# Optimization experiments

Hardware: AMD Instinct MI355X
Metric: run time of the kernel (lower is better)

## Reference

```python
import jax, jax.numpy as jnp
import numpy as np

N = 50000        # n_nodes
E = 640000       # n_edges
D = 128          # d_model (in_dim == out_dim)
H = 8            # num_heads
DH = D // H      # head dim = 16
EPS = 1e-5


def _batchnorm(x, g, b):
    # BatchNorm1d, training-mode batch statistics (biased variance)
    mu = jnp.mean(x, axis=0)
    var = jnp.mean((x - mu) ** 2, axis=0)
    return (x - mu) * jax.lax.rsqrt(var + EPS) * g + b


def setup_inputs() -> dict:
    key = jax.random.key(0)
    ks = jax.random.split(key, 16)
    s = 0.05
    h = jax.random.normal(ks[0], (N, D), jnp.float32)
    src = jax.random.randint(ks[1], (E,), 0, N)
    # guarantee every node has >= 1 incoming edge (avoids z == 0)
    dst = jnp.concatenate([jnp.arange(N), jax.random.randint(ks[2], (E - N,), 0, N)])
    return {
        "h": h,
        "src": src,
        "dst": dst,
        "WQ": jax.random.normal(ks[3], (D, D), jnp.float32) * s,
        "WK": jax.random.normal(ks[4], (D, D), jnp.float32) * s,
        "WV": jax.random.normal(ks[5], (D, D), jnp.float32) * s,
        "WO": jax.random.normal(ks[6], (D, D), jnp.float32) * s,
        "bO": jnp.zeros((D,), jnp.float32),
        "W1": jax.random.normal(ks[7], (2 * D, D), jnp.float32) * s,
        "b1": jnp.zeros((2 * D,), jnp.float32),
        "W2": jax.random.normal(ks[8], (D, 2 * D), jnp.float32) * s,
        "b2": jnp.zeros((D,), jnp.float32),
        "bn1_g": jnp.ones((D,), jnp.float32),
        "bn1_b": jnp.zeros((D,), jnp.float32),
        "bn2_g": jnp.ones((D,), jnp.float32),
        "bn2_b": jnp.zeros((D,), jnp.float32),
    }


def reference(h, src, dst, WQ, WK, WV, WO, bO, W1, b1, W2, b2, bn1_g, bn1_b, bn2_g, bn2_b):
    n = h.shape[0]
    # projections -> [N, H, DH]
    Q = (h @ WQ.T).reshape(n, H, DH)
    K = (h @ WK.T).reshape(n, H, DH)
    V = (h @ WV.T).reshape(n, H, DH)
    # per-edge score: sum(K[src] * Q[dst]) -> [E, H]; clamp/exp (scaled_exp)
    score = jnp.sum(K[src] * Q[dst], axis=-1) / np.sqrt(DH)
    score = jnp.exp(jnp.clip(score, -5.0, 5.0))
    # scatter-sum weighted values and normalizers to destination nodes
    wV = jax.ops.segment_sum(V[src] * score[..., None], dst, num_segments=n)  # [N,H,DH]
    z = jax.ops.segment_sum(score, dst, num_segments=n)                       # [N,H]
    attn = (wV / z[..., None]).reshape(n, D)
    # O projection + residual + BN1
    h1 = _batchnorm(h + (attn @ WO.T + bO), bn1_g, bn1_b)
    # FFN + residual + BN2
    f = jax.nn.relu(h1 @ W1.T + b1) @ W2.T + b2
    return _batchnorm(h1 + f, bn2_g, bn2_b)
```

## Files before the change

### kernel.cpp

```cpp
#include <hip/hip_runtime.h>
#include <math.h>


#define ND128 16384
typedef _Float16 f16;
typedef __attribute__((ext_vector_type(8))) _Float16 h8;
typedef __attribute__((ext_vector_type(4))) _Float16 h4;
typedef __attribute__((ext_vector_type(2))) _Float16 h2;
typedef __attribute__((ext_vector_type(4))) float f4;

__global__ __launch_bounds__(256) void k_prep(
    const float* __restrict__ h, f16* __restrict__ hb,
    const float* __restrict__ WQ, const float* __restrict__ WK,
    const float* __restrict__ WV, const float* __restrict__ WO,
    const float* __restrict__ W2,
    f16* __restrict__ Wqb, f16* __restrict__ Wkb,
    f16* __restrict__ Wvb, f16* __restrict__ Wob, f16* __restrict__ W2b,
    float* __restrict__ bn, int* __restrict__ cursor, int N)
{
    const int slab = blockIdx.x;
    const int tid = threadIdx.x;
    if (tid < 128) {
        int ci = slab * 128 + tid;
        if (ci < N) cursor[ci] = 0;
    }
    if (slab == 6) { bn[tid] = 0.f; bn[tid + 256] = 0.f; }
#pragma unroll
    for (int it = 0; it < 8; ++it) {
        int cid = it * 256 + tid;
        int lane = cid & 63;
        int m = (cid >> 6) & 7;
        int kb = cid >> 9;
        int row = slab * 128 + m * 16 + (lane & 15);
        int col = kb * 32 + (lane >> 4) * 8;
        f16 o8[8];
        if (row < N) {
            const float* p = h + (size_t)row * 128 + col;
            float4 f0 = *(const float4*)p;
            float4 f1 = *(const float4*)(p + 4);
            o8[0] = (f16)f0.x; o8[1] = (f16)f0.y; o8[2] = (f16)f0.z; o8[3] = (f16)f0.w;
            o8[4] = (f16)f1.x; o8[5] = (f16)f1.y; o8[6] = (f16)f1.z; o8[7] = (f16)f1.w;
        } else {
#pragma unroll
            for (int j = 0; j < 8; ++j) o8[j] = (f16)0.f;
        }
        *(h8*)(hb + (size_t)slab * ND128 + (size_t)cid * 8) = *(const h8*)o8;
    }
    if (slab < 6) {
        const float* Wsrc; f16* dst; int K, base;
        if (slab < 4) {
            Wsrc = slab == 0 ? WQ : slab == 1 ? WK : slab == 2 ? WV : WO;
            dst  = slab == 0 ? Wqb : slab == 1 ? Wkb : slab == 2 ? Wvb : Wob;
            K = 128; base = 0;
        } else {
            Wsrc = W2; dst = W2b; K = 256; base = (slab - 4) * 2048;
        }
#pragma unroll
        for (int it = 0; it < 8; ++it) {
            int cid = base + it * 256 + tid;
            int lane = cid & 63;
            int kb, nt;
            if (K == 128) { kb = (cid >> 6) & 3; nt = cid >> 8; }
            else          { kb = (cid >> 6) & 7; nt = cid >> 9; }
            int row = nt * 16 + (lane & 15);
            int col = kb * 32 + (lane >> 4) * 8;
            const float* p = Wsrc + (size_t)row * K + col;
            f16 o8[8];
#pragma unroll
            for (int j = 0; j < 8; ++j) o8[j] = (f16)p[j];
            *(h8*)(dst + (size_t)cid * 8) = *(const h8*)o8;
        }
    }
}

__global__ __launch_bounds__(256) void k_qkv(
    const f16* __restrict__ hb, const f16* __restrict__ Wqb,
    const f16* __restrict__ Wkb, const f16* __restrict__ Wvb,
    f16* __restrict__ Qb, f16* __restrict__ Kb, f16* __restrict__ Vb, int N)
{
    const int slab = blockIdx.x;
    const int w = threadIdx.x >> 6, lane = threadIdx.x & 63;
    const f16* __restrict__ Wb = blockIdx.y == 0 ? Wqb : blockIdx.y == 1 ? Wkb : Wvb;
    f16* __restrict__ Ob = blockIdx.y == 0 ? Qb : blockIdx.y == 1 ? Kb : Vb;
    const f16* A = hb + (size_t)slab * ND128;

    h8 bfr[2][4];
#pragma unroll
    for (int nt = 0; nt < 2; ++nt)
#pragma unroll
        for (int kb = 0; kb < 4; ++kb)
            bfr[nt][kb] = *(const h8*)(Wb + (size_t)(((2 * w + nt) * 4 + kb) * 64 + lane) * 8);

    f4 acc[8][2];
    f4 zero = {0.f, 0.f, 0.f, 0.f};
#pragma unroll
    for (int m = 0; m < 8; ++m) { acc[m][0] = zero; acc[m][1] = zero; }

#pragma unroll
    for (int m = 0; m < 8; ++m) {
#pragma unroll
        for (int kb = 0; kb < 4; ++kb) {
            h8 a = *(const h8*)(A + (size_t)((kb * 8 + m) * 64 + lane) * 8);
            acc[m][0] = __builtin_amdgcn_mfma_f32_16x16x32_f16(bfr[0][kb], a, acc[m][0], 0, 0, 0);
            acc[m][1] = __builtin_amdgcn_mfma_f32_16x16x32_f16(bfr[1][kb], a, acc[m][1], 0, 0, 0);
        }
    }

    const int rl = lane & 15, quad = lane >> 4;
#pragma unroll
    for (int m = 0; m < 8; ++m) {
        int gr = slab * 128 + m * 16 + rl;
        if (gr < N) {
#pragma unroll
            for (int nt = 0; nt < 2; ++nt) {
                h4 o;
                o[0] = (f16)acc[m][nt][0]; o[1] = (f16)acc[m][nt][1];
                o[2] = (f16)acc[m][nt][2]; o[3] = (f16)acc[m][nt][3];
                *(h4*)(Ob + (size_t)gr * 128 + w * 32 + nt * 16 + quad * 4) = o;
            }
        }
    }
}

__global__ __launch_bounds__(256) void k_hist(
    const int* __restrict__ dst, int* __restrict__ cursor, int E)
{
    int e = blockIdx.x * 256 + threadIdx.x;
    if (e < E) atomicAdd(&cursor[dst[e]], 1);
}

__global__ __launch_bounds__(256) void k_scanA(
    const int* __restrict__ cnt, int* __restrict__ bsum, int N)
{
    const int t = threadIdx.x;
    int base = blockIdx.x * 2048 + t * 8;
    int s = 0;
#pragma unroll
    for (int j = 0; j < 8; ++j) {
        int idx = base + j;
        if (idx < N) s += cnt[idx];
    }
#pragma unroll
    for (int off = 32; off; off >>= 1) s += __shfl_down(s, off, 64);
    __shared__ int ws4[4];
    if ((t & 63) == 0) ws4[t >> 6] = s;
    __syncthreads();
    if (t == 0) bsum[blockIdx.x] = ws4[0] + ws4[1] + ws4[2] + ws4[3];
}

__global__ __launch_bounds__(256) void k_scanC(
    const int* __restrict__ cnt, const int* __restrict__ bsum,
    int* __restrict__ rowptr, int* __restrict__ cursor, int N, int nsb)
{
    const int t = threadIdx.x, b = blockIdx.x;
    __shared__ int sboff;
    if (t == 0) {
        int r = 0;
        for (int i2 = 0; i2 < b; ++i2) r += bsum[i2];
        sboff = r;
    }
    if (t == 64 && b == nsb - 1) {
        int r = 0;
        for (int i2 = 0; i2 < nsb; ++i2) r += bsum[i2];
        rowptr[N] = r;
    }
    int base = b * 2048 + t * 8;
    int loc[8];
    int s = 0;
#pragma unroll
    for (int j = 0; j < 8; ++j) {
        int idx = base + j;
        loc[j] = (idx < N) ? cnt[idx] : 0;
        s += loc[j];
    }
    __shared__ int part[256];
    part[t] = s;
    __syncthreads();
    for (int off = 1; off < 256; off <<= 1) {
        int v = (t >= off) ? part[t - off] : 0;
        __syncthreads();
        part[t] += v;
        __syncthreads();
    }
    int run = sboff + (t ? part[t - 1] : 0);
#pragma unroll
    for (int j = 0; j < 8; ++j) {
        int idx = base + j;
        if (idx < N) { rowptr[idx] = run; cursor[idx] = run; run += loc[j]; }
    }
}

__global__ __launch_bounds__(256) void k_scatter(
    const int* __restrict__ src, const int* __restrict__ dst,
    int* __restrict__ cursor, int* __restrict__ csr_src, int E)
{
    int e = blockIdx.x * 256 + threadIdx.x;
    if (e < E) {
        int pos = atomicAdd(&cursor[dst[e]], 1);
        csr_src[pos] = src[e];
    }
}

__global__ __launch_bounds__(256) void k_attn(
    const f16* __restrict__ Qb, const f16* __restrict__ Kb,
    const f16* __restrict__ Vb,
    const int* __restrict__ rowptr, const int* __restrict__ csr_src,
    f16* __restrict__ attnf, int N)
{
    const int node = blockIdx.x * 4 + (threadIdx.x >> 6);
    const int lane = threadIdx.x & 63;
    if (node >= N) return;
    const int beg = rowptr[node], end = rowptr[node + 1];
    const h2 q2 = ((const h2*)(Qb + (size_t)node * 128))[lane];
    h2 accA = {(f16)0.f, (f16)0.f};
    h2 accB = {(f16)0.f, (f16)0.f};
    float zA = 0.f, zB = 0.f;
    int i = beg;
    for (; i + 3 < end; i += 4) {
        int s0 = csr_src[i], s1 = csr_src[i + 1];
        int s2 = csr_src[i + 2], s3 = csr_src[i + 3];
        h2 k0 = ((const h2*)(Kb + (size_t)s0 * 128))[lane];
        h2 k1 = ((const h2*)(Kb + (size_t)s1 * 128))[lane];
        h2 k2 = ((const h2*)(Kb + (size_t)s2 * 128))[lane];
        h2 k3 = ((const h2*)(Kb + (size_t)s3 * 128))[lane];
        h2 v0 = ((const h2*)(Vb + (size_t)s0 * 128))[lane];
        h2 v1 = ((const h2*)(Vb + (size_t)s1 * 128))[lane];
        h2 v2 = ((const h2*)(Vb + (size_t)s2 * 128))[lane];
        h2 v3 = ((const h2*)(Vb + (size_t)s3 * 128))[lane];
        float p0 = __builtin_amdgcn_fdot2(q2, k0, 0.f, false);
        float p1 = __builtin_amdgcn_fdot2(q2, k1, 0.f, false);
        float p2 = __builtin_amdgcn_fdot2(q2, k2, 0.f, false);
        float p3 = __builtin_amdgcn_fdot2(q2, k3, 0.f, false);
        p0 += __shfl_xor(p0, 4, 8); p1 += __shfl_xor(p1, 4, 8);
        p2 += __shfl_xor(p2, 4, 8); p3 += __shfl_xor(p3, 4, 8);
        p0 += __shfl_xor(p0, 2, 8); p1 += __shfl_xor(p1, 2, 8);
        p2 += __shfl_xor(p2, 2, 8); p3 += __shfl_xor(p3, 2, 8);
        p0 += __shfl_xor(p0, 1, 8); p1 += __shfl_xor(p1, 1, 8);
        p2 += __shfl_xor(p2, 1, 8); p3 += __shfl_xor(p3, 1, 8);
        float sc0 = __expf(fminf(fmaxf(p0 * 0.25f, -5.f), 5.f));
        float sc1 = __expf(fminf(fmaxf(p1 * 0.25f, -5.f), 5.f));
        float sc2 = __expf(fminf(fmaxf(p2 * 0.25f, -5.f), 5.f));
        float sc3 = __expf(fminf(fmaxf(p3 * 0.25f, -5.f), 5.f));
        h2 h0 = {(f16)sc0, (f16)sc0}, h1v = {(f16)sc1, (f16)sc1};
        h2 h2v = {(f16)sc2, (f16)sc2}, h3 = {(f16)sc3, (f16)sc3};
        accA = v0 * h0 + accA;  accB = v1 * h1v + accB;
        accA = v2 * h2v + accA; accB = v3 * h3 + accB;
        zA += sc0 + sc2; zB += sc1 + sc3;
    }
    for (; i < end; ++i) {
        int s0 = csr_src[i];
        h2 k0 = ((const h2*)(Kb + (size_t)s0 * 128))[lane];
        h2 v0 = ((const h2*)(Vb + (size_t)s0 * 128))[lane];
        float p0 = __builtin_amdgcn_fdot2(q2, k0, 0.f, false);
        p0 += __shfl_xor(p0, 4, 8); p0 += __shfl_xor(p0, 2, 8); p0 += __shfl_xor(p0, 1, 8);
        float sc0 = __expf(fminf(fmaxf(p0 * 0.25f, -5.f), 5.f));
        h2 h0 = {(f16)sc0, (f16)sc0};
        accA = v0 * h0 + accA;
        zA += sc0;
    }
    h2 acc2 = accA + accB;
    float z = zA + zB;
    float inv = 1.f / z;
    h2 o2 = {(f16)((float)acc2.x * inv), (f16)((float)acc2.y * inv)};
    int slab = node >> 7, m = (node >> 4) & 7, lr = node & 15;
    int kb = lane >> 4, quad2 = (lane & 15) >> 2, j = (lane & 3) * 2;
    *(h2*)(attnf + (size_t)slab * ND128 +
           (size_t)(((kb * 8 + m) * 64 + lr + 16 * quad2) * 8 + j)) = o2;
}

__global__ __launch_bounds__(256) void k_oproj(
    const f16* __restrict__ attnf, const f16* __restrict__ Wob,
    const float* __restrict__ h, const float* __restrict__ bO,
    f16* __restrict__ t1b, float* __restrict__ bn, int N)
{
    __shared__ float csum[128], csq[128];
    const int tid = threadIdx.x, slab = blockIdx.x;
    const int w = tid >> 6, lane = tid & 63;
    if (tid < 128) { csum[tid] = 0.f; csq[tid] = 0.f; }
    __syncthreads();
    const f16* A = attnf + (size_t)slab * ND128;

    h8 bfr[2][4];
#pragma unroll
    for (int nt = 0; nt < 2; ++nt)
#pragma unroll
        for (int kb = 0; kb < 4; ++kb)
            bfr[nt][kb] = *(const h8*)(Wob + (size_t)(((2 * w + nt) * 4 + kb) * 64 + lane) * 8);

    f4 acc[8][2];
    f4 zero = {0.f, 0.f, 0.f, 0.f};
#pragma unroll
    for (int m = 0; m < 8; ++m) { acc[m][0] = zero; acc[m][1] = zero; }
#pragma unroll
    for (int m = 0; m < 8; ++m) {
#pragma unroll
        for (int kb = 0; kb < 4; ++kb) {
            h8 a = *(const h8*)(A + (size_t)((kb * 8 + m) * 64 + lane) * 8);
            acc[m][0] = __builtin_amdgcn_mfma_f32_16x16x32_f16(bfr[0][kb], a, acc[m][0], 0, 0, 0);
            acc[m][1] = __builtin_amdgcn_mfma_f32_16x16x32_f16(bfr[1][kb], a, acc[m][1], 0, 0, 0);
        }
    }

    const int rl = lane & 15, quad = lane >> 4;
    float4 bo[2];
#pragma unroll
    for (int nt = 0; nt < 2; ++nt)
        bo[nt] = *(const float4*)(bO + w * 32 + nt * 16 + quad * 4);
    float pcs[2][4], pcq[2][4];
#pragma unroll
    for (int nt = 0; nt < 2; ++nt)
#pragma unroll
        for (int r = 0; r < 4; ++r) { pcs[nt][r] = 0.f; pcq[nt][r] = 0.f; }

#pragma unroll
    for (int m = 0; m < 8; ++m) {
        int gr = slab * 128 + m * 16 + rl;
        if (gr < N) {
#pragma unroll
            for (int nt = 0; nt < 2; ++nt) {
                int col0 = w * 32 + nt * 16 + quad * 4;
                float4 hv = *(const float4*)(h + (size_t)gr * 128 + col0);
                float v0 = acc[m][nt][0] + hv.x + bo[nt].x;
                float v1 = acc[m][nt][1] + hv.y + bo[nt].y;
                float v2 = acc[m][nt][2] + hv.z + bo[nt].z;
                float v3 = acc[m][nt][3] + hv.w + bo[nt].w;
                h4 o; o[0] = (f16)v0; o[1] = (f16)v1; o[2] = (f16)v2; o[3] = (f16)v3;
                *(h4*)(t1b + (size_t)slab * ND128 +
                       (size_t)(((w * 8 + m) * 64 + (nt * 2 + (quad >> 1)) * 16 + rl) * 8 +
                                (quad & 1) * 4)) = o;
                pcs[nt][0] += v0; pcq[nt][0] += v0 * v0;
                pcs[nt][1] += v1; pcq[nt][1] += v1 * v1;
                pcs[nt][2] += v2; pcq[nt][2] += v2 * v2;
                pcs[nt][3] += v3; pcq[nt][3] += v3 * v3;
            }
        }
    }
#pragma unroll
    for (int nt = 0; nt < 2; ++nt)
#pragma unroll
        for (int r = 0; r < 4; ++r) {
            float s = pcs[nt][r], q = pcq[nt][r];
            s += __shfl_xor(s, 8, 16); q += __shfl_xor(q, 8, 16);
            s += __shfl_xor(s, 4, 16); q += __shfl_xor(q, 4, 16);
            s += __shfl_xor(s, 2, 16); q += __shfl_xor(q, 2, 16);
            s += __shfl_xor(s, 1, 16); q += __shfl_xor(q, 1, 16);
            if (rl == 0) {
                int cl = w * 32 + nt * 16 + quad * 4 + r;
                atomicAdd(&csum[cl], s);
                atomicAdd(&csq[cl], q);
            }
        }
    __syncthreads();
    if (tid < 128) {
        atomicAdd(bn + tid, csum[tid]);
        atomicAdd(bn + 128 + tid, csq[tid]);
    }
}

__global__ __launch_bounds__(128) void k_fold1(
    const float* __restrict__ bn, const float* __restrict__ g1,
    const float* __restrict__ bb1, const float* __restrict__ W1,
    const float* __restrict__ b1, f16* __restrict__ W1b,
    float* __restrict__ badj, float* __restrict__ sfold,
    float* __restrict__ bfold, int N)
{
    const int o = blockIdx.x, i = threadIdx.x;
    float invN = 1.f / (float)N;
    float mu = bn[i] * invN;
    float var = bn[128 + i] * invN - mu * mu;
    float s = g1[i] * rsqrtf(var + 1e-5f);
    float bb = bb1[i] - mu * s;
    if (o == 0) { sfold[i] = s; bfold[i] = bb; }
    float wv = W1[(size_t)o * 128 + i];
    __shared__ float red[128];
    red[i] = wv * bb;
    const int nt = o >> 4, lanelow = o & 15;
    const int kb = i >> 5, quad = (i >> 3) & 3, j = i & 7;
    W1b[(size_t)(((nt * 4 + kb) * 64 + lanelow + 16 * quad) * 8 + j)] = (f16)(wv * s);
    __syncthreads();
#pragma unroll
    for (int off = 64; off; off >>= 1) {
        if (i < off) red[i] += red[i + off];
        __syncthreads();
    }
    if (i == 0) badj[o] = b1[o] + red[0];
}

__global__ __launch_bounds__(256) void k_ffn1(
    const f16* __restrict__ t1b, const f16* __restrict__ W1b,
    const float* __restrict__ badj, f16* __restrict__ ub, int N)
{
    const int slab = blockIdx.x, ch = blockIdx.y;
    const int w = threadIdx.x >> 6, lane = threadIdx.x & 63;
    const f16* A = t1b + (size_t)slab * ND128;

    h8 bfr[2][4];
#pragma unroll
    for (int nt = 0; nt < 2; ++nt)
#pragma unroll
        for (int kb = 0; kb < 4; ++kb) {
            int ntg = ch * 8 + 2 * w + nt;
            bfr[nt][kb] = *(const h8*)(W1b + (size_t)((ntg * 4 + kb) * 64 + lane) * 8);
        }

    f4 acc[8][2];
    f4 zero = {0.f, 0.f, 0.f, 0.f};
#pragma unroll
    for (int m = 0; m < 8; ++m) { acc[m][0] = zero; acc[m][1] = zero; }
#pragma unroll
    for (int m = 0; m < 8; ++m) {
#pragma unroll
        for (int kb = 0; kb < 4; ++kb) {
            h8 a = *(const h8*)(A + (size_t)((kb * 8 + m) * 64 + lane) * 8);
            acc[m][0] = __builtin_amdgcn_mfma_f32_16x16x32_f16(bfr[0][kb], a, acc[m][0], 0, 0, 0);
            acc[m][1] = __builtin_amdgcn_mfma_f32_16x16x32_f16(bfr[1][kb], a, acc[m][1], 0, 0, 0);
        }
    }

    const int rl = lane & 15, quad = lane >> 4;
    const int kbu = ch * 4 + w;
    float4 ba[2];
#pragma unroll
    for (int nt = 0; nt < 2; ++nt)
        ba[nt] = *(const float4*)(badj + ch * 128 + w * 32 + nt * 16 + quad * 4);
#pragma unroll
    for (int m = 0; m < 8; ++m) {
        int gr = slab * 128 + m * 16 + rl;
        if (gr < N) {
#pragma unroll
            for (int nt = 0; nt < 2; ++nt) {
                h4 o;
                o[0] = (f16)fmaxf(acc[m][nt][0] + ba[nt].x, 0.f);
                o[1] = (f16)fmaxf(acc[m][nt][1] + ba[nt].y, 0.f);
                o[2] = (f16)fmaxf(acc[m][nt][2] + ba[nt].z, 0.f);
                o[3] = (f16)fmaxf(acc[m][nt][3] + ba[nt].w, 0.f);
                *(h4*)(ub + (size_t)slab * 32768 +
                       (size_t)(((kbu * 8 + m) * 64 + (nt * 2 + (quad >> 1)) * 16 + rl) * 8 +
                                (quad & 1) * 4)) = o;
            }
        }
    }
}

__global__ __launch_bounds__(256) void k_ffn2(
    const f16* __restrict__ ub, const f16* __restrict__ W2b,
    const f16* __restrict__ t1b,
    const float* __restrict__ sfold, const float* __restrict__ bfold,
    const float* __restrict__ b2, float* __restrict__ out,
    float* __restrict__ bn, int N)
{
    __shared__ float csum[128], csq[128], sS[128], sB[128];
    const int tid = threadIdx.x, slab = blockIdx.x;
    const int w = tid >> 6, lane = tid & 63;
    if (tid < 128) {
        csum[tid] = 0.f; csq[tid] = 0.f;
        sS[tid] = sfold[tid]; sB[tid] = bfold[tid] + b2[tid];
    }
    __syncthreads();
    const f16* A = ub + (size_t)slab * 32768;
    const f16* T1 = t1b + (size_t)slab * ND128;

    h8 bfr[2][8];
#pragma unroll
    for (int nt = 0; nt < 2; ++nt)
#pragma unroll
        for (int kb = 0; kb < 8; ++kb)
            bfr[nt][kb] = *(const h8*)(W2b + (size_t)(((2 * w + nt) * 8 + kb) * 64 + lane) * 8);

    f4 acc[8][2];
    f4 zero = {0.f, 0.f, 0.f, 0.f};
#pragma unroll
    for (int m = 0; m < 8; ++m) { acc[m][0] = zero; acc[m][1] = zero; }
#pragma unroll
    for (int m = 0; m < 8; ++m) {
#pragma unroll
        for (int kb = 0; kb < 8; ++kb) {
            h8 a = *(const h8*)(A + (size_t)((kb * 8 + m) * 64 + lane) * 8);
            acc[m][0] = __builtin_amdgcn_mfma_f32_16x16x32_f16(bfr[0][kb], a, acc[m][0], 0, 0, 0);
            acc[m][1] = __builtin_amdgcn_mfma_f32_16x16x32_f16(bfr[1][kb], a, acc[m][1], 0, 0, 0);
        }
    }

    const int rl = lane & 15, quad = lane >> 4;
    float pcs[2][4], pcq[2][4];
#pragma unroll
    for (int nt = 0; nt < 2; ++nt)
#pragma unroll
        for (int r = 0; r < 4; ++r) { pcs[nt][r] = 0.f; pcq[nt][r] = 0.f; }

#pragma unroll
    for (int m = 0; m < 8; ++m) {
        int gr = slab * 128 + m * 16 + rl;
        if (gr < N) {
#pragma unroll
            for (int nt = 0; nt < 2; ++nt) {
                int col0 = w * 32 + nt * 16 + quad * 4;
                h4 t1v = *(const h4*)(T1 +
                    (size_t)(((w * 8 + m) * 64 + (nt * 2 + (quad >> 1)) * 16 + rl) * 8 +
                             (quad & 1) * 4));
                float4 ss = *(const float4*)&sS[col0];
                float4 sb = *(const float4*)&sB[col0];
                float4 o;
                o.x = acc[m][nt][0] + fmaf(ss.x, (float)t1v[0], sb.x);
                o.y = acc[m][nt][1] + fmaf(ss.y, (float)t1v[1], sb.y);
                o.z = acc[m][nt][2] + fmaf(ss.z, (float)t1v[2], sb.z);
                o.w = acc[m][nt][3] + fmaf(ss.w, (float)t1v[3], sb.w);
                *(float4*)(out + (size_t)gr * 128 + col0) = o;
                pcs[nt][0] += o.x; pcq[nt][0] += o.x * o.x;
                pcs[nt][1] += o.y; pcq[nt][1] += o.y * o.y;
                pcs[nt][2] += o.z; pcq[nt][2] += o.z * o.z;
                pcs[nt][3] += o.w; pcq[nt][3] += o.w * o.w;
            }
        }
    }
#pragma unroll
    for (int nt = 0; nt < 2; ++nt)
#pragma unroll
        for (int r = 0; r < 4; ++r) {
            float s = pcs[nt][r], q = pcq[nt][r];
            s += __shfl_xor(s, 8, 16); q += __shfl_xor(q, 8, 16);
            s += __shfl_xor(s, 4, 16); q += __shfl_xor(q, 4, 16);
            s += __shfl_xor(s, 2, 16); q += __shfl_xor(q, 2, 16);
            s += __shfl_xor(s, 1, 16); q += __shfl_xor(q, 1, 16);
            if (rl == 0) {
                int cl = w * 32 + nt * 16 + quad * 4 + r;
                atomicAdd(&csum[cl], s);
                atomicAdd(&csq[cl], q);
            }
        }
    __syncthreads();
    if (tid < 128) {
        atomicAdd(bn + 256 + tid, csum[tid]);
        atomicAdd(bn + 384 + tid, csq[tid]);
    }
}

__global__ __launch_bounds__(256) void k_bn2(
    float* __restrict__ out, const float* __restrict__ bn,
    const float* __restrict__ g2, const float* __restrict__ bb2, int N)
{
    __shared__ float sS[128], sB[128];
    const int tid = threadIdx.x;
    if (tid < 128) {
        float invN = 1.f / (float)N;
        float mu = bn[256 + tid] * invN;
        float var = bn[384 + tid] * invN - mu * mu;
        float scl = g2[tid] * rsqrtf(var + 1e-5f);
        sS[tid] = scl;
        sB[tid] = bb2[tid] - mu * scl;
    }
    __syncthreads();
    size_t idx = (size_t)blockIdx.x * 256 + tid;
    size_t total = (size_t)N * 32;
    if (idx < total) {
        int c0 = (int)((idx * 4) & 127);
        float4 v = *(const float4*)(out + idx * 4);
        v.x = fmaf(v.x, sS[c0 + 0], sB[c0 + 0]);
        v.y = fmaf(v.y, sS[c0 + 1], sB[c0 + 1]);
        v.z = fmaf(v.z, sS[c0 + 2], sB[c0 + 2]);
        v.w = fmaf(v.w, sS[c0 + 3], sB[c0 + 3]);
        *(float4*)(out + idx * 4) = v;
    }
}

extern "C" void kernel_launch(void* const* d_in, const int* in_sizes, int n_in,
                              void* d_out, int out_size, void* d_ws, size_t ws_size,
                              hipStream_t stream)
{
    const float* h   = (const float*)d_in[0];
    const int*   src = (const int*)d_in[1];
    const int*   dst = (const int*)d_in[2];
    const float* WQ  = (const float*)d_in[3];
    const float* WK  = (const float*)d_in[4];
    const float* WV  = (const float*)d_in[5];
    const float* WO  = (const float*)d_in[6];
    const float* bO  = (const float*)d_in[7];
    const float* W1  = (const float*)d_in[8];
    const float* b1  = (const float*)d_in[9];
    const float* W2  = (const float*)d_in[10];
    const float* b2  = (const float*)d_in[11];
    const float* g1  = (const float*)d_in[12];
    const float* bb1 = (const float*)d_in[13];
    const float* g2  = (const float*)d_in[14];
    const float* bb2 = (const float*)d_in[15];
    float* out = (float*)d_out;

    int N = in_sizes[0] / 128;
    int E = in_sizes[1];
    const int slabs = (N + 127) / 128;
    const int nsb = (N + 2047) / 2048;
    const size_t B1 = (size_t)slabs * 32768;

    char* Wp = (char*)d_ws;
    f16* hb  = (f16*)Wp;
    f16* Qb  = (f16*)(Wp + B1);
    f16* Kb  = (f16*)(Wp + 2 * B1);
    f16* Vb  = (f16*)(Wp + 3 * B1);
    f16* t1b = (f16*)(Wp + 3 * B1);
    f16* ub  = (f16*)(Wp + B1);
    const size_t base = 4 * B1;
    f16* Wqb = (f16*)(Wp + base);
    f16* Wkb = (f16*)(Wp + base + 32768);
    f16* Wvb = (f16*)(Wp + base + 65536);
    f16* Wob = (f16*)(Wp + base + 98304);
    f16* W1b = (f16*)(Wp + base + 131072);
    f16* W2b = (f16*)(Wp + base + 196608);
    float* badj  = (float*)(Wp + base + 262144);
    float* sfold = (float*)(Wp + base + 263168);
    float* bfold = (float*)(Wp + base + 263680);
    float* bn    = (float*)(Wp + base + 264192);
    int* cursor  = (int*)(Wp + base + 266240);
    int* rowptr  = (int*)(Wp + base + 266240 + (size_t)N * 4);
    int* csr     = (int*)(Wp + base + 266240 + (size_t)N * 8 + 8);
    int* bsum    = (int*)((char*)csr + (size_t)E * 4);

    k_prep<<<slabs, 256, 0, stream>>>(h, hb, WQ, WK, WV, WO, W2,
                                      Wqb, Wkb, Wvb, Wob, W2b, bn, cursor, N);
    k_qkv<<<dim3(slabs, 3), 256, 0, stream>>>(hb, Wqb, Wkb, Wvb, Qb, Kb, Vb, N);
    k_hist<<<(E + 255) / 256, 256, 0, stream>>>(dst, cursor, E);
    k_scanA<<<nsb, 256, 0, stream>>>(cursor, bsum, N);
    k_scanC<<<nsb, 256, 0, stream>>>(cursor, bsum, rowptr, cursor, N, nsb);
    k_scatter<<<(E + 255) / 256, 256, 0, stream>>>(src, dst, cursor, csr, E);
    k_attn<<<(N + 3) / 4, 256, 0, stream>>>(Qb, Kb, Vb, rowptr, csr, hb, N);
    k_oproj<<<slabs, 256, 0, stream>>>(hb, Wob, h, bO, t1b, bn, N);
    k_fold1<<<256, 128, 0, stream>>>(bn, g1, bb1, W1, b1, W1b, badj, sfold, bfold, N);
    k_ffn1<<<dim3(slabs, 2), 256, 0, stream>>>(t1b, W1b, badj, ub, N);
    k_ffn2<<<slabs, 256, 0, stream>>>(ub, W2b, t1b, sfold, bfold, b2, out, bn, N);
    k_bn2<<<(int)(((size_t)N * 32 + 255) / 256), 256, 0, stream>>>(out, bn, g2, bb2, N);
}
```

Before: 331.9 us.

## Store K and V in fp8 and fuse h conversion into QKV projection

K and V are now written as fp8 (e4m3) and decoded to fp32 inside the edge-gather attention kernel. This halves the bytes fetched per gathered edge, which is where the random-access memory traffic is concentrated. The h-to-fp16 conversion moves into a single fused QKV kernel that loads each slab of h once and computes all three projections, removing the separate hb buffer and the three-way grid. The cost is reduced precision on K and V, which may push error past tolerance, plus extra decode arithmetic in the attention loop.

```diff
diff --git a/kernel.cpp b/kernel.cpp
--- a/kernel.cpp
+++ b/kernel.cpp
@@ -8,115 +8,177 @@
 typedef __attribute__((ext_vector_type(4))) _Float16 h4;
 typedef __attribute__((ext_vector_type(2))) _Float16 h2;
 typedef __attribute__((ext_vector_type(4))) float f4;
+typedef __attribute__((ext_vector_type(2))) float ff2;
+
+__device__ __forceinline__ ff2 fp8x2_dec(unsigned v) {
+#if __has_builtin(__builtin_amdgcn_cvt_pk_f32_fp8)
+    return __builtin_amdgcn_cvt_pk_f32_fp8((int)v, false);
+#else
+    ff2 r;
+    unsigned b0 = v & 0xffu, b1 = (v >> 8) & 0xffu;
+    {
+        unsigned e = (b0 >> 3) & 15u, m = b0 & 7u;
+        float x = e ? __uint_as_float(((e + 120u) << 23) | (m << 20)) : (float)m * 0.001953125f;
+        r.x = (b0 & 0x80u) ? -x : x;
+    }
+    {
+        unsigned e = (b1 >> 3) & 15u, m = b1 & 7u;
+        float x = e ? __uint_as_float(((e + 120u) << 23) | (m << 20)) : (float)m * 0.001953125f;
+        r.y = (b1 & 0x80u) ? -x : x;
+    }
+    return r;
+#endif
+}
+
+#if !__has_builtin(__builtin_amdgcn_cvt_pk_fp8_f32)
+__device__ __forceinline__ unsigned char fp8_1(float f) {
+    float a = fabsf(f);
+    unsigned sg = (__float_as_uint(f) >> 31) << 7;
+    if (a >= 448.f) return (unsigned char)(sg | 0x7E);
+    if (a < 0.0009765625f) return (unsigned char)sg;
+    int E; float m = frexpf(a, &E);
+    if (E - 1 < -6) {
+        int q = (int)rintf(a * 512.f);
+        if (q > 7) return (unsigned char)(sg | 0x08);
+        return (unsigned char)(sg | q);
+    }
+    int q = (int)rintf(m * 16.f);
+    if (q == 16) { q = 8; E += 1; }
+    int Ef = E - 1 + 7;
+    if (Ef > 15) return (unsigned char)(sg | 0x7E);
+    return (unsigned char)(sg | (Ef << 3) | (q - 8));
+}
+#endif
+
+__device__ __forceinline__ unsigned fp8_pack4(float a0, float a1, float a2, float a3) {
+#if __has_builtin(__builtin_amdgcn_cvt_pk_fp8_f32)
+    int pk = __builtin_amdgcn_cvt_pk_fp8_f32(a0, a1, 0, false);
+    pk = __builtin_amdgcn_cvt_pk_fp8_f32(a2, a3, pk, true);
+    return (unsigned)pk;
+#else
+    return (unsigned)fp8_1(a0) | ((unsigned)fp8_1(a1) << 8) |
+           ((unsigned)fp8_1(a2) << 16) | ((unsigned)fp8_1(a3) << 24);
+#endif
+}
 
 __global__ __launch_bounds__(256) void k_prep(
-    const float* __restrict__ h, f16* __restrict__ hb,
     const float* __restrict__ WQ, const float* __restrict__ WK,
     const float* __restrict__ WV, const float* __restrict__ WO,
     const float* __restrict__ W2,
     f16* __restrict__ Wqb, f16* __restrict__ Wkb,
     f16* __restrict__ Wvb, f16* __restrict__ Wob, f16* __restrict__ W2b,
-    float* __restrict__ bn, int* __restrict__ cursor, int N)
-{
-    const int slab = blockIdx.x;
-    const int tid = threadIdx.x;
+    float* __restrict__ bn)
+{
+    const int b = blockIdx.x, tid = threadIdx.x;
+    if (b == 0) { bn[tid] = 0.f; bn[tid + 256] = 0.f; }
+    const float* Wsrc; f16* dst; int K, base;
+    if (b < 4) {
+        Wsrc = b == 0 ? WQ : b == 1 ? WK : b == 2 ? WV : WO;
+        dst  = b == 0 ? Wqb : b == 1 ? Wkb : b == 2 ? Wvb : Wob;
+        K = 128; base = 0;
+    } else {
+        Wsrc = W2; dst = W2b; K = 256; base = (b - 4) * 2048;
+    }
+#pragma unroll
+    for (int it = 0; it < 8; ++it) {
+        int cid = base + it * 256 + tid;
+        int lane = cid & 63;
+        int kb, nt;
+        if (K == 128) { kb = (cid >> 6) & 3; nt = cid >> 8; }
+        else          { kb = (cid >> 6) & 7; nt = cid >> 9; }
+        int row = nt * 16 + (lane & 15);
+        int col = kb * 32 + (lane >> 4) * 8;
+        const float* p = Wsrc + (size_t)row * K + col;
+        f16 o8[8];
+#pragma unroll
+        for (int j = 0; j < 8; ++j) o8[j] = (f16)p[j];
+        *(h8*)(dst + (size_t)cid * 8) = *(const h8*)o8;
+    }
+}
+
+__global__ __launch_bounds__(256) void k_qkvF(
+    const float* __restrict__ h,
+    const f16* __restrict__ Wqb, const f16* __restrict__ Wkb, const f16* __restrict__ Wvb,
+    f16* __restrict__ Qb, unsigned char* __restrict__ Kb8, unsigned char* __restrict__ Vb8,
+    int* __restrict__ cursor, int N)
+{
+    const int slab = blockIdx.x, tid = threadIdx.x;
+    const int w = tid >> 6, lane = tid & 63;
+    const int rl = lane & 15, quad = lane >> 4;
     if (tid < 128) {
         int ci = slab * 128 + tid;
         if (ci < N) cursor[ci] = 0;
     }
-    if (slab == 6) { bn[tid] = 0.f; bn[tid + 256] = 0.f; }
-#pragma unroll
-    for (int it = 0; it < 8; ++it) {
-        int cid = it * 256 + tid;
-        int lane = cid & 63;
-        int m = (cid >> 6) & 7;
-        int kb = cid >> 9;
-        int row = slab * 128 + m * 16 + (lane & 15);
-        int col = kb * 32 + (lane >> 4) * 8;
-        f16 o8[8];
-        if (row < N) {
-            const float* p = h + (size_t)row * 128 + col;
-            float4 f0 = *(const float4*)p;
-            float4 f1 = *(const float4*)(p + 4);
-            o8[0] = (f16)f0.x; o8[1] = (f16)f0.y; o8[2] = (f16)f0.z; o8[3] = (f16)f0.w;
-            o8[4] = (f16)f1.x; o8[5] = (f16)f1.y; o8[6] = (f16)f1.z; o8[7] = (f16)f1.w;
+
+    h8 afr[8][4];
+#pragma unroll
+    for (int m = 0; m < 8; ++m) {
+        int row = slab * 128 + m * 16 + rl;
+#pragma unroll
+        for (int kb = 0; kb < 4; ++kb) {
+            h8 a;
+            if (row < N) {
+                const float* p = h + (size_t)row * 128 + kb * 32 + quad * 8;
+                float4 f0 = *(const float4*)p;
+                float4 f1 = *(const float4*)(p + 4);
+                a[0] = (f16)f0.x; a[1] = (f16)f0.y; a[2] = (f16)f0.z; a[3] = (f16)f0.w;
+                a[4] = (f16)f1.x; a[5] = (f16)f1.y; a[6] = (f16)f1.z; a[7] = (f16)f1.w;
+            } else {
+#pragma unroll
+                for (int j = 0; j < 8; ++j) a[j] = (f16)0.f;
+            }
+            afr[m][kb] = a;
+        }
+    }
+
+    for (int oidx = 0; oidx < 3; ++oidx) {
+        const f16* __restrict__ Wb = oidx == 0 ? Wqb : oidx == 1 ? Wkb : Wvb;
+        h8 bfr[2][4];
+#pragma unroll
+        for (int nt = 0; nt < 2; ++nt)
+#pragma unroll
+            for (int kb = 0; kb < 4; ++kb)
+                bfr[nt][kb] = *(const h8*)(Wb + (size_t)(((2 * w + nt) * 4 + kb) * 64 + lane) * 8);
+
+        f4 acc[8][2];
+        f4 zero = {0.f, 0.f, 0.f, 0.f};
+#pragma unroll
+        for (int m = 0; m < 8; ++m) { acc[m][0] = zero; acc[m][1] = zero; }
+#pragma unroll
+        for (int m = 0; m < 8; ++m)
+#pragma unroll
+            for (int kb = 0; kb < 4; ++kb) {
+                acc[m][0] = __builtin_amdgcn_mfma_f32_16x16x32_f16(bfr[0][kb], afr[m][kb], acc[m][0], 0, 0, 0);
+                acc[m][1] = __builtin_amdgcn_mfma_f32_16x16x32_f16(bfr[1][kb], afr[m][kb], acc[m][1], 0, 0, 0);
+            }
+
+        if (oidx == 0) {
+#pragma unroll
+            for (int m = 0; m < 8; ++m) {
+                int gr = slab * 128 + m * 16 + rl;
+                if (gr < N) {
+#pragma unroll
+                    for (int nt = 0; nt < 2; ++nt) {
+                        h4 o;
+                        o[0] = (f16)acc[m][nt][0]; o[1] = (f16)acc[m][nt][1];
+                        o[2] = (f16)acc[m][nt][2]; o[3] = (f16)acc[m][nt][3];
+                        *(h4*)(Qb + (size_t)gr * 128 + w * 32 + nt * 16 + quad * 4) = o;
+                    }
+                }
+            }
         } else {
-#pragma unroll
-            for (int j = 0; j < 8; ++j) o8[j] = (f16)0.f;
-        }
-        *(h8*)(hb + (size_t)slab * ND128 + (size_t)cid * 8) = *(const h8*)o8;
-    }
-    if (slab < 6) {
-        const float* Wsrc; f16* dst; int K, base;
-        if (slab < 4) {
-            Wsrc = slab == 0 ? WQ : slab == 1 ? WK : slab == 2 ? WV : WO;
-            dst  = slab == 0 ? Wqb : slab == 1 ? Wkb : slab == 2 ? Wvb : Wob;
-            K = 128; base = 0;
-        } else {
-            Wsrc = W2; dst = W2b; K = 256; base = (slab - 4) * 2048;
-        }
-#pragma unroll
-        for (int it = 0; it < 8; ++it) {
-            int cid = base + it * 256 + tid;
-            int lane = cid & 63;
-            int kb, nt;
-            if (K == 128) { kb = (cid >> 6) & 3; nt = cid >> 8; }
-            else          { kb = (cid >> 6) & 7; nt = cid >> 9; }
-            int row = nt * 16 + (lane & 15);
-            int col = kb * 32 + (lane >> 4) * 8;
-            const float* p = Wsrc + (size_t)row * K + col;
-            f16 o8[8];
-#pragma unroll
-            for (int j = 0; j < 8; ++j) o8[j] = (f16)p[j];
-            *(h8*)(dst + (size_t)cid * 8) = *(const h8*)o8;
-        }
-    }
-}
-
-__global__ __launch_bounds__(256) void k_qkv(
-    const f16* __restrict__ hb, const f16* __restrict__ Wqb,
-    const f16* __restrict__ Wkb, const f16* __restrict__ Wvb,
-    f16* __restrict__ Qb, f16* __restrict__ Kb, f16* __restrict__ Vb, int N)
-{
-    const int slab = blockIdx.x;
-    const int w = threadIdx.x >> 6, lane = threadIdx.x & 63;
-    const f16* __restrict__ Wb = blockIdx.y == 0 ? Wqb : blockIdx.y == 1 ? Wkb : Wvb;
-    f16* __restrict__ Ob = blockIdx.y == 0 ? Qb : blockIdx.y == 1 ? Kb : Vb;
-    const f16* A = hb + (size_t)slab * ND128;
-
-    h8 bfr[2][4];
-#pragma unroll
-    for (int nt = 0; nt < 2; ++nt)
-#pragma unroll
-        for (int kb = 0; kb < 4; ++kb)
-            bfr[nt][kb] = *(const h8*)(Wb + (size_t)(((2 * w + nt) * 4 + kb) * 64 + lane) * 8);
-
-    f4 acc[8][2];
-    f4 zero = {0.f, 0.f, 0.f, 0.f};
-#pragma unroll
-    for (int m = 0; m < 8; ++m) { acc[m][0] = zero; acc[m][1] = zero; }
-
-#pragma unroll
-    for (int m = 0; m < 8; ++m) {
-#pragma unroll
-        for (int kb = 0; kb < 4; ++kb) {
-            h8 a = *(const h8*)(A + (size_t)((kb * 8 + m) * 64 + lane) * 8);
-            acc[m][0] = __builtin_amdgcn_mfma_f32_16x16x32_f16(bfr[0][kb], a, acc[m][0], 0, 0, 0);
-            acc[m][1] = __builtin_amdgcn_mfma_f32_16x16x32_f16(bfr[1][kb], a, acc[m][1], 0, 0, 0);
-        }
-    }
-
-    const int rl = lane & 15, quad = lane >> 4;
-#pragma unroll
-    for (int m = 0; m < 8; ++m) {
-        int gr = slab * 128 + m * 16 + rl;
-        if (gr < N) {
-#pragma unroll
-            for (int nt = 0; nt < 2; ++nt) {
-                h4 o;
-                o[0] = (f16)acc[m][nt][0]; o[1] = (f16)acc[m][nt][1];
-                o[2] = (f16)acc[m][nt][2]; o[3] = (f16)acc[m][nt][3];
-                *(h4*)(Ob + (size_t)gr * 128 + w * 32 + nt * 16 + quad * 4) = o;
+            unsigned char* __restrict__ O8 = oidx == 1 ? Kb8 : Vb8;
+#pragma unroll
+            for (int m = 0; m < 8; ++m) {
+                int gr = slab * 128 + m * 16 + rl;
+                if (gr < N) {
+#pragma unroll
+                    for (int nt = 0; nt < 2; ++nt) {
+                        unsigned pk = fp8_pack4(acc[m][nt][0], acc[m][nt][1],
+                                                acc[m][nt][2], acc[m][nt][3]);
+                        *(unsigned*)(O8 + (size_t)gr * 128 + w * 32 + nt * 16 + quad * 4) = pk;
+                    }
+                }
             }
         }
     }
@@ -202,8 +264,8 @@
 }
 
 __global__ __launch_bounds__(256) void k_attn(
-    const f16* __restrict__ Qb, const f16* __restrict__ Kb,
-    const f16* __restrict__ Vb,
+    const f16* __restrict__ Qb, const unsigned char* __restrict__ Kb8,
+    const unsigned char* __restrict__ Vb8,
     const int* __restrict__ rowptr, const int* __restrict__ csr_src,
     f16* __restrict__ attnf, int N)
 {
@@ -212,25 +274,26 @@
     if (node >= N) return;
     const int beg = rowptr[node], end = rowptr[node + 1];
     const h2 q2 = ((const h2*)(Qb + (size_t)node * 128))[lane];
-    h2 accA = {(f16)0.f, (f16)0.f};
-    h2 accB = {(f16)0.f, (f16)0.f};
-    float zA = 0.f, zB = 0.f;
+    const float qx = (float)q2[0], qy = (float)q2[1];
+    float axA = 0.f, ayA = 0.f, axB = 0.f, ayB = 0.f, zA = 0.f, zB = 0.f;
     int i = beg;
     for (; i + 3 < end; i += 4) {
         int s0 = csr_src[i], s1 = csr_src[i + 1];
         int s2 = csr_src[i + 2], s3 = csr_src[i + 3];
-        h2 k0 = ((const h2*)(Kb + (size_t)s0 * 128))[lane];
-        h2 k1 = ((const h2*)(Kb + (size_t)s1 * 128))[lane];
-        h2 k2 = ((const h2*)(Kb + (size_t)s2 * 128))[lane];
-        h2 k3 = ((const h2*)(Kb + (size_t)s3 * 128))[lane];
-        h2 v0 = ((const h2*)(Vb + (size_t)s0 * 128))[lane];
-        h2 v1 = ((const h2*)(Vb + (size_t)s1 * 128))[lane];
-        h2 v2 = ((const h2*)(Vb + (size_t)s2 * 128))[lane];
-        h2 v3 = ((const h2*)(Vb + (size_t)s3 * 128))[lane];
-        float p0 = __builtin_amdgcn_fdot2(q2, k0, 0.f, false);
-        float p1 = __builtin_amdgcn_fdot2(q2, k1, 0.f, false);
-        float p2 = __builtin_amdgcn_fdot2(q2, k2, 0.f, false);
-        float p3 = __builtin_amdgcn_fdot2(q2, k3, 0.f, false);
+        unsigned k0 = *(const unsigned short*)(Kb8 + (size_t)s0 * 128 + 2 * lane);
+        unsigned k1 = *(const unsigned short*)(Kb8 + (size_t)s1 * 128 + 2 * lane);
+        unsigned k2 = *(const unsigned short*)(Kb8 + (size_t)s2 * 128 + 2 * lane);
+        unsigned k3 = *(const unsigned short*)(Kb8 + (size_t)s3 * 128 + 2 * lane);
+        unsigned v0 = *(const unsigned short*)(Vb8 + (size_t)s0 * 128 + 2 * lane);
+        unsigned v1 = *(const unsigned short*)(Vb8 + (size_t)s1 * 128 + 2 * lane);
+        unsigned v2 = *(const unsigned short*)(Vb8 + (size_t)s2 * 128 + 2 * lane);
+        unsigned v3 = *(const unsigned short*)(Vb8 + (size_t)s3 * 128 + 2 * lane);
+        ff2 kf0 = fp8x2_dec(k0), kf1 = fp8x2_dec(k1);
+        ff2 kf2 = fp8x2_dec(k2), kf3 = fp8x2_dec(k3);
+        float p0 = fmaf(qx, kf0.x, qy * kf0.y);
+        float p1 = fmaf(qx, kf1.x, qy * kf1.y);
+        float p2 = fmaf(qx, kf2.x, qy * kf2.y);
+        float p3 = fmaf(qx, kf3.x, qy * kf3.y);
         p0 += __shfl_xor(p0, 4, 8); p1 += __shfl_xor(p1, 4, 8);
         p2 += __shfl_xor(p2, 4, 8); p3 += __shfl_xor(p3, 4, 8);
         p0 += __shfl_xor(p0, 2, 8); p1 += __shfl_xor(p1, 2, 8);
@@ -241,27 +304,30 @@
         float sc1 = __expf(fminf(fmaxf(p1 * 0.25f, -5.f), 5.f));
         float sc2 = __expf(fminf(fmaxf(p2 * 0.25f, -5.f), 5.f));
         float sc3 = __expf(fminf(fmaxf(p3 * 0.25f, -5.f), 5.f));
-        h2 h0 = {(f16)sc0, (f16)sc0}, h1v = {(f16)sc1, (f16)sc1};
-        h2 h2v = {(f16)sc2, (f16)sc2}, h3 = {(f16)sc3, (f16)sc3};
-        accA = v0 * h0 + accA;  accB = v1 * h1v + accB;
-        accA = v2 * h2v + accA; accB = v3 * h3 + accB;
+        ff2 vf0 = fp8x2_dec(v0), vf1 = fp8x2_dec(v1);
+        ff2 vf2 = fp8x2_dec(v2), vf3 = fp8x2_dec(v3);
+        axA = fmaf(vf0.x, sc0, axA); ayA = fmaf(vf0.y, sc0, ayA);
+        axB = fmaf(vf1.x, sc1, axB); ayB = fmaf(vf1.y, sc1, ayB);
+        axA = fmaf(vf2.x, sc2, axA); ayA = fmaf(vf2.y, sc2, ayA);
+        axB = fmaf(vf3.x, sc3, axB); ayB = fmaf(vf3.y, sc3, ayB);
         zA += sc0 + sc2; zB += sc1 + sc3;
     }
     for (; i < end; ++i) {
         int s0 = csr_src[i];
-        h2 k0 = ((const h2*)(Kb + (size_t)s0 * 128))[lane];
-        h2 v0 = ((const h2*)(Vb + (size_t)s0 * 128))[lane];
-        float p0 = __builtin_amdgcn_fdot2(q2, k0, 0.f, false);
+        unsigned k0 = *(const unsigned short*)(Kb8 + (size_t)s0 * 128 + 2 * lane);
+        unsigned v0 = *(const unsigned short*)(Vb8 + (size_t)s0 * 128 + 2 * lane);
+        ff2 kf0 = fp8x2_dec(k0);
+        float p0 = fmaf(qx, kf0.x, qy * kf0.y);
         p0 += __shfl_xor(p0, 4, 8); p0 += __shfl_xor(p0, 2, 8); p0 += __shfl_xor(p0, 1, 8);
         float sc0 = __expf(fminf(fmaxf(p0 * 0.25f, -5.f), 5.f));
-        h2 h0 = {(f16)sc0, (f16)sc0};
-        accA = v0 * h0 + accA;
+        ff2 vf0 = fp8x2_dec(v0);
+        axA = fmaf(vf0.x, sc0, axA); ayA = fmaf(vf0.y, sc0, ayA);
         zA += sc0;
     }
-    h2 acc2 = accA + accB;
-    float z = zA + zB;
-    float inv = 1.f / z;
-    h2 o2 = {(f16)((float)acc2.x * inv), (f16)((float)acc2.y * inv)};
+    float inv = 1.f / (zA + zB);
+    h2 o2;
+    o2[0] = (f16)((axA + axB) * inv);
+    o2[1] = (f16)((ayA + ayB) * inv);
     int slab = node >> 7, m = (node >> 4) & 7, lr = node & 15;
     int kb = lane >> 4, quad2 = (lane & 15) >> 2, j = (lane & 3) * 2;
     *(h2*)(attnf + (size_t)slab * ND128 +
@@ -592,12 +658,12 @@
     const size_t B1 = (size_t)slabs * 32768;
 
     char* Wp = (char*)d_ws;
-    f16* hb  = (f16*)Wp;
+    f16* attnf = (f16*)Wp;
     f16* Qb  = (f16*)(Wp + B1);
-    f16* Kb  = (f16*)(Wp + 2 * B1);
-    f16* Vb  = (f16*)(Wp + 3 * B1);
+    unsigned char* Kb8 = (unsigned char*)(Wp + 2 * B1);
+    unsigned char* Vb8 = (unsigned char*)(Wp + 2 * B1 + B1 / 2);
+    f16* ub  = (f16*)(Wp + B1);
     f16* t1b = (f16*)(Wp + 3 * B1);
-    f16* ub  = (f16*)(Wp + B1);
     const size_t base = 4 * B1;
     f16* Wqb = (f16*)(Wp + base);
     f16* Wkb = (f16*)(Wp + base + 32768);
@@ -614,15 +680,14 @@
     int* csr     = (int*)(Wp + base + 266240 + (size_t)N * 8 + 8);
     int* bsum    = (int*)((char*)csr + (size_t)E * 4);
 
-    k_prep<<<slabs, 256, 0, stream>>>(h, hb, WQ, WK, WV, WO, W2,
-                                      Wqb, Wkb, Wvb, Wob, W2b, bn, cursor, N);
-    k_qkv<<<dim3(slabs, 3), 256, 0, stream>>>(hb, Wqb, Wkb, Wvb, Qb, Kb, Vb, N);
+    k_prep<<<6, 256, 0, stream>>>(WQ, WK, WV, WO, W2, Wqb, Wkb, Wvb, Wob, W2b, bn);
+    k_qkvF<<<slabs, 256, 0, stream>>>(h, Wqb, Wkb, Wvb, Qb, Kb8, Vb8, cursor, N);
     k_hist<<<(E + 255) / 256, 256, 0, stream>>>(dst, cursor, E);
     k_scanA<<<nsb, 256, 0, stream>>>(cursor, bsum, N);
     k_scanC<<<nsb, 256, 0, stream>>>(cursor, bsum, rowptr, cursor, N, nsb);
     k_scatter<<<(E + 255) / 256, 256, 0, stream>>>(src, dst, cursor, csr, E);
-    k_attn<<<(N + 3) / 4, 256, 0, stream>>>(Qb, Kb, Vb, rowptr, csr, hb, N);
-    k_oproj<<<slabs, 256, 0, stream>>>(hb, Wob, h, bO, t1b, bn, N);
+    k_attn<<<(N + 3) / 4, 256, 0, stream>>>(Qb, Kb8, Vb8, rowptr, csr, attnf, N);
+    k_oproj<<<slabs, 256, 0, stream>>>(attnf, Wob, h, bO, t1b, bn, N);
     k_fold1<<<256, 128, 0, stream>>>(bn, g1, bb1, W1, b1, W1b, badj, sfold, bfold, N);
     k_ffn1<<<dim3(slabs, 2), 256, 0, stream>>>(t1b, W1b, badj, ub, N);
     k_ffn2<<<slabs, 256, 0, stream>>>(ub, W2b, t1b, sfold, bfold, b2, out, bn, N);
```

Result: no change. 332.8 us (+0.3%).
